# Kernel optimization log

Measured on AMD Instinct MI355X. Metric: run time of the kernel, lower is better.

## Reference

```python
import jax, jax.numpy as jnp
import numpy as np

N = 100000   # nodes
E = 1600000  # edges
D = 128      # in_dim
H = 128      # hidden_dim
C = 40       # num_classes
EPS = 1e-5   # LayerNorm eps (torch default)


def setup_inputs() -> dict:
    key = jax.random.key(0)
    ks = jax.random.split(key, 16)
    x = jax.random.normal(ks[0], (N, D), dtype=jnp.float32)
    edge_index = jax.random.randint(ks[1], (2, E), 0, N, dtype=jnp.int64)
    s = 1.0 / np.sqrt(D)
    inp = {"x": x, "edge_index": edge_index}
    # 3 GCN layers: weight [in, H], bias [H]; LayerNorm gamma/beta [H]
    for i in range(3):
        inp[f"W{i}"] = jax.random.normal(ks[2 + i], (D if i == 0 else H, H), dtype=jnp.float32) * s
        inp[f"b{i}"] = jnp.zeros((H,), jnp.float32)
        inp[f"g{i}"] = jnp.ones((H,), jnp.float32)
        inp[f"be{i}"] = jnp.zeros((H,), jnp.float32)
    inp["Wc"] = jax.random.normal(ks[10], (H, C), dtype=jnp.float32) * (1.0 / np.sqrt(H))
    inp["bc"] = jnp.zeros((C,), jnp.float32)
    return inp


def _layer_norm(h, g, b):
    mu = jnp.mean(h, axis=-1, keepdims=True)
    var = jnp.var(h, axis=-1, keepdims=True)  # biased, matches torch
    return (h - mu) * jax.lax.rsqrt(var + EPS) * g + b


def _gcn_conv(x, W, b, src, dst, enorm, dinv2):
    # GCNConv: D^{-1/2}(A+I)D^{-1/2} X W + b (self-loops handled analytically)
    h = x @ W                                   # [N, H]
    agg = jax.ops.segment_sum(h[src] * enorm[:, None], dst, num_segments=N)
    return agg + h * dinv2[:, None] + b


def reference(x, edge_index, W0, b0, g0, be0, W1, b1, g1, be1, W2, b2, g2, be2, Wc, bc):
    src, dst = edge_index[0], edge_index[1]
    # degree with self-loops (GCNConv adds self-loops by default)
    deg = jnp.zeros((N,), x.dtype).at[dst].add(1.0) + 1.0
    dinv = jax.lax.rsqrt(deg)
    enorm = dinv[src] * dinv[dst]               # per-edge normalization
    dinv2 = dinv * dinv                         # self-loop normalization

    Ws, bs, gs, bes = (W0, W1, W2), (b0, b1, b2), (g0, g1, g2), (be0, be1, be2)
    for i in range(3):
        x_in = x
        x = _gcn_conv(x, Ws[i], bs[i], src, dst, enorm, dinv2)
        x = _layer_norm(x, gs[i], bes[i])
        x = jax.nn.elu(x)
        if i > 0:
            x = x + x_in
        # dropout: eval mode / p=0 -> identity
    return x @ Wc + bc
```

## Files before the change

### kernel.cpp

```cpp
#include <hip/hip_runtime.h>
#include <math.h>

#define N_NODES 100000
#define N_EDGES 1600000
#define DIM     128
#define NCLS    40
#define NBUCK   196
#define P1_CH   4096
#define P1_GRID 391

typedef _Float16 f16x8 __attribute__((ext_vector_type(8)));
typedef _Float16 f16x2 __attribute__((ext_vector_type(2)));
typedef float    f32x4 __attribute__((ext_vector_type(4)));

__device__ inline unsigned short f16bits(float f) {
    union { _Float16 h; unsigned short u; } cv;
    cv.h = (_Float16)f;
    return cv.u;
}
__device__ inline f16x2 as_h2(unsigned u) {
    union { unsigned u; f16x2 h; } cv;
    cv.u = u;
    return cv.h;
}
__device__ inline unsigned as_u(f16x2 h) {
    union { f16x2 h; unsigned u; } cv;
    cv.h = h;
    return cv.u;
}
__device__ inline unsigned pack_h2(float lo, float hi) {
    f16x2 h;
    h.x = (_Float16)lo;
    h.y = (_Float16)hi;
    return as_u(h);
}

__global__ __launch_bounds__(256) void setup_misc(const float* __restrict__ W0,
                                                  const float* __restrict__ W1,
                                                  const float* __restrict__ W2,
                                                  const float* __restrict__ Wc,
                                                  unsigned short* __restrict__ Wsw0,
                                                  unsigned short* __restrict__ Wsw1,
                                                  unsigned short* __restrict__ Wsw2,
                                                  unsigned short* __restrict__ Wcsw,
                                                  int* __restrict__ bcnt) {
    int blk = blockIdx.x;
    if (blk < 192) {
        const float* W = (blk < 64) ? W0 : (blk < 128) ? W1 : W2;
        unsigned short* Wsw = (blk < 64) ? Wsw0 : (blk < 128) ? Wsw1 : Wsw2;
        int o = (blk & 63) * 256 + threadIdx.x;
        int f = o >> 9;
        int l = (o >> 3) & 63;
        int j = o & 7;
        int n = f >> 2;
        int s = f & 3;
        int k = s * 32 + (l >> 4) * 8 + j;
        int c = (l & 15) * 8 + n;
        Wsw[o] = f16bits(W[k * DIM + c]);
    } else if (blk < 216) {
        int o = (blk - 192) * 256 + threadIdx.x;
        int f = o >> 9;
        int l = (o >> 3) & 63;
        int j = o & 7;
        int n = f >> 2;
        int s = f & 3;
        int k = s * 32 + (l >> 4) * 8 + j;
        int c = (l & 15) * 3 + n;
        Wcsw[o] = (c < NCLS) ? f16bits(Wc[k * NCLS + c]) : (unsigned short)0;
    } else {
        bcnt[threadIdx.x] = 0;
    }
}

__global__ __launch_bounds__(256) void bhist(const int* __restrict__ ei,
                                             int* __restrict__ bcnt) {
    __shared__ int h[256];
    const int t  = threadIdx.x;
    const int e0 = blockIdx.x * P1_CH;
    const int cnt = min(P1_CH, N_EDGES - e0);
    h[t] = 0;
    __syncthreads();
    for (int i = t; i < cnt; i += 256)
        atomicAdd(&h[ei[N_EDGES + e0 + i] >> 9], 1);
    __syncthreads();
    if (h[t]) atomicAdd(&bcnt[t], h[t]);
}

__global__ __launch_bounds__(256) void bscan(const int* __restrict__ bcnt,
                                             int* __restrict__ bbase,
                                             int* __restrict__ bcur) {
    __shared__ int s[256];
    int t = threadIdx.x;
    s[t] = (t < NBUCK) ? bcnt[t] : 0;
    __syncthreads();
    for (int off = 1; off < 256; off <<= 1) {
        int x = (t >= off) ? s[t - off] : 0;
        __syncthreads();
        s[t] += x;
        __syncthreads();
    }
    int excl = (t == 0) ? 0 : s[t - 1];
    if (t < NBUCK) {
        bbase[t] = excl;
        bcur[t]  = excl;
    }
    if (t == 0) bbase[NBUCK] = N_EDGES;
}

__global__ __launch_bounds__(256) void bucket_p1(const int* __restrict__ ei,
                                                 int* __restrict__ bcur,
                                                 int2* __restrict__ tmp) {
    __shared__ int  hist[256];
    __shared__ int  lscan[256];
    __shared__ int  rank[256];
    __shared__ int  gbase[256];
    __shared__ int2 stage[P1_CH];
    const int t  = threadIdx.x;
    const int e0 = blockIdx.x * P1_CH;
    const int cnt = min(P1_CH, N_EDGES - e0);

    hist[t] = 0;
    __syncthreads();

    int2 ed[16];
#pragma unroll
    for (int i = 0; i < 16; ++i) {
        int idx = t + i * 256;
        if (idx < cnt) {
            int s = ei[e0 + idx];
            int d = ei[N_EDGES + e0 + idx];
            ed[i] = make_int2(s, d);
            atomicAdd(&hist[d >> 9], 1);
        }
    }
    __syncthreads();

    int hv = hist[t];
    lscan[t] = hv;
    __syncthreads();
    for (int off = 1; off < 256; off <<= 1) {
        int x = (t >= off) ? lscan[t - off] : 0;
        __syncthreads();
        lscan[t] += x;
        __syncthreads();
    }
    int excl = (t == 0) ? 0 : lscan[t - 1];
    __syncthreads();
    lscan[t] = excl;
    rank[t]  = excl;
    if (hv > 0) gbase[t] = atomicAdd(&bcur[t], hv);
    __syncthreads();

#pragma unroll
    for (int i = 0; i < 16; ++i) {
        int idx = t + i * 256;
        if (idx < cnt) {
            int b = ed[i].y >> 9;
            int p = atomicAdd(&rank[b], 1);
            stage[p] = ed[i];
        }
    }
    __syncthreads();

    for (int p = t; p < cnt; p += 256) {
        int2 v = stage[p];
        int b = v.y >> 9;
        tmp[gbase[b] + (p - lscan[b])] = v;
    }
}

__global__ __launch_bounds__(256) void bucket_p2a(const int2* __restrict__ tmp,
                                                  const int* __restrict__ bbase,
                                                  int* __restrict__ rowptr,
                                                  float* __restrict__ dinv) {
    __shared__ int cnt[512];
    __shared__ int pscan[256];
    const int t  = threadIdx.x;
    const int b  = blockIdx.x;
    const int d0 = b << 9;
    const int dend = min(d0 + 512, N_NODES);
    const int nn = dend - d0;

    cnt[t] = 0;
    cnt[t + 256] = 0;
    __syncthreads();

    const int beg = bbase[b];
    const int end = bbase[b + 1];
    for (int idx = beg + t; idx < end; idx += 256)
        atomicAdd(&cnt[tmp[idx].y - d0], 1);
    __syncthreads();

    int c0 = cnt[2 * t];
    int c1 = cnt[2 * t + 1];
    pscan[t] = c0 + c1;
    __syncthreads();
    for (int off = 1; off < 256; off <<= 1) {
        int x = (t >= off) ? pscan[t - off] : 0;
        __syncthreads();
        pscan[t] += x;
        __syncthreads();
    }
    int excl = (t == 0) ? 0 : pscan[t - 1];
    if (2 * t < nn) {
        rowptr[d0 + 2 * t] = beg + excl;
        dinv[d0 + 2 * t]   = rsqrtf((float)c0 + 1.0f);
    }
    if (2 * t + 1 < nn) {
        rowptr[d0 + 2 * t + 1] = beg + excl + c0;
        dinv[d0 + 2 * t + 1]   = rsqrtf((float)c1 + 1.0f);
    }
    if (b == NBUCK - 1 && t == 0) rowptr[N_NODES] = N_EDGES;
}

__global__ __launch_bounds__(256) void bucket_p2b(const int2* __restrict__ tmp,
                                                  const int* __restrict__ rowptr,
                                                  const float* __restrict__ dinv,
                                                  int2* __restrict__ rec) {
    __shared__ int cur[512];
    const int t  = threadIdx.x;
    const int b  = blockIdx.x;
    const int d0 = b << 9;
    const int dend = min(d0 + 512, N_NODES);
    const int nn = dend - d0;

    for (int i = t; i < nn; i += 256) cur[i] = rowptr[d0 + i];
    __syncthreads();

    const int beg = rowptr[d0];
    const int end = rowptr[dend];
    for (int idx = beg + t; idx < end; idx += 256) {
        int2 v = tmp[idx];
        int s = v.x, d = v.y;
        int pos = atomicAdd(&cur[d - d0], 1);
        unsigned short wb = f16bits(dinv[s] * dinv[d]);
        rec[pos] = make_int2(s << 8, (int)((unsigned)wb | ((unsigned)wb << 16)));
    }
}

__global__ __launch_bounds__(256, 2) void gemm_mfma_f(const float* __restrict__ X,
                                                      const unsigned short* __restrict__ Wsw,
                                                      unsigned short* __restrict__ H) {
    __shared__ unsigned short wlds[32 * 512];
    const int tid   = threadIdx.x;
    const int lane  = tid & 63;
    const int wave  = tid >> 6;
    const int row0w = blockIdx.x * 128 + wave * 32;
    const int m = lane & 15;
    const int q = lane >> 4;

    {
        const uint4* srcp = (const uint4*)Wsw;
        uint4*       dstp = (uint4*)wlds;
#pragma unroll
        for (int i = 0; i < 8; ++i) dstp[tid + i * 256] = srcp[tid + i * 256];
    }
    __syncthreads();

    f16x8 wf[32];
#pragma unroll
    for (int f = 0; f < 32; ++f)
        wf[f] = *(const f16x8*)(wlds + (f << 9) + lane * 8);

    f16x8 af[2][4];
#pragma unroll
    for (int ggr = 0; ggr < 2; ++ggr) {
        int r = row0w + ggr * 16 + m;
        if (r >= N_NODES) r = N_NODES - 1;
        const float* xp = X + (size_t)r * DIM + q * 8;
#pragma unroll
        for (int s = 0; s < 4; ++s) {
            float4 x0 = *(const float4*)(xp + s * 32);
            float4 x1 = *(const float4*)(xp + s * 32 + 4);
            f16x8 v;
            v[0] = (_Float16)x0.x; v[1] = (_Float16)x0.y;
            v[2] = (_Float16)x0.z; v[3] = (_Float16)x0.w;
            v[4] = (_Float16)x1.x; v[5] = (_Float16)x1.y;
            v[6] = (_Float16)x1.z; v[7] = (_Float16)x1.w;
            af[ggr][s] = v;
        }
    }

    f32x4 acc[2][8];
    f32x4 z = {0.f, 0.f, 0.f, 0.f};
#pragma unroll
    for (int ggr = 0; ggr < 2; ++ggr)
#pragma unroll
        for (int n = 0; n < 8; ++n) acc[ggr][n] = z;

#pragma unroll
    for (int s = 0; s < 4; ++s)
#pragma unroll
        for (int n = 0; n < 8; ++n) {
            acc[0][n] = __builtin_amdgcn_mfma_f32_16x16x32_f16(af[0][s], wf[n * 4 + s], acc[0][n], 0, 0, 0);
            acc[1][n] = __builtin_amdgcn_mfma_f32_16x16x32_f16(af[1][s], wf[n * 4 + s], acc[1][n], 0, 0, 0);
        }

#pragma unroll
    for (int ggr = 0; ggr < 2; ++ggr)
#pragma unroll
        for (int j = 0; j < 4; ++j) {
            int row = row0w + ggr * 16 + q * 4 + j;
            if (row < N_NODES) {
                uint4 o;
                o.x = pack_h2(acc[ggr][0][j], acc[ggr][1][j]);
                o.y = pack_h2(acc[ggr][2][j], acc[ggr][3][j]);
                o.z = pack_h2(acc[ggr][4][j], acc[ggr][5][j]);
                o.w = pack_h2(acc[ggr][6][j], acc[ggr][7][j]);
                *(uint4*)(H + (size_t)row * DIM + m * 8) = o;
            }
        }
}

__global__ __launch_bounds__(256, 2) void gemm_mfma_h(const unsigned short* __restrict__ Xh,
                                                      const unsigned short* __restrict__ Wsw,
                                                      unsigned short* __restrict__ H) {
    __shared__ unsigned short wlds[32 * 512];
    const int tid   = threadIdx.x;
    const int lane  = tid & 63;
    const int wave  = tid >> 6;
    const int row0w = blockIdx.x * 128 + wave * 32;
    const int m = lane & 15;
    const int q = lane >> 4;

    {
        const uint4* srcp = (const uint4*)Wsw;
        uint4*       dstp = (uint4*)wlds;
#pragma unroll
        for (int i = 0; i < 8; ++i) dstp[tid + i * 256] = srcp[tid + i * 256];
    }
    __syncthreads();

    f16x8 wf[32];
#pragma unroll
    for (int f = 0; f < 32; ++f)
        wf[f] = *(const f16x8*)(wlds + (f << 9) + lane * 8);

    f16x8 af[2][4];
#pragma unroll
    for (int ggr = 0; ggr < 2; ++ggr) {
        int r = row0w + ggr * 16 + m;
        if (r >= N_NODES) r = N_NODES - 1;
        const unsigned short* xp = Xh + (size_t)r * DIM + q * 8;
#pragma unroll
        for (int s = 0; s < 4; ++s) af[ggr][s] = *(const f16x8*)(xp + s * 32);
    }

    f32x4 acc[2][8];
    f32x4 z = {0.f, 0.f, 0.f, 0.f};
#pragma unroll
    for (int ggr = 0; ggr < 2; ++ggr)
#pragma unroll
        for (int n = 0; n < 8; ++n) acc[ggr][n] = z;

#pragma unroll
    for (int s = 0; s < 4; ++s)
#pragma unroll
        for (int n = 0; n < 8; ++n) {
            acc[0][n] = __builtin_amdgcn_mfma_f32_16x16x32_f16(af[0][s], wf[n * 4 + s], acc[0][n], 0, 0, 0);
            acc[1][n] = __builtin_amdgcn_mfma_f32_16x16x32_f16(af[1][s], wf[n * 4 + s], acc[1][n], 0, 0, 0);
        }

#pragma unroll
    for (int ggr = 0; ggr < 2; ++ggr)
#pragma unroll
        for (int j = 0; j < 4; ++j) {
            int row = row0w + ggr * 16 + q * 4 + j;
            if (row < N_NODES) {
                uint4 o;
                o.x = pack_h2(acc[ggr][0][j], acc[ggr][1][j]);
                o.y = pack_h2(acc[ggr][2][j], acc[ggr][3][j]);
                o.z = pack_h2(acc[ggr][4][j], acc[ggr][5][j]);
                o.w = pack_h2(acc[ggr][6][j], acc[ggr][7][j]);
                *(uint4*)(H + (size_t)row * DIM + m * 8) = o;
            }
        }
}

__global__ __launch_bounds__(256) void agg_ln(const unsigned short* __restrict__ Hh,
                                              const unsigned short* __restrict__ xin,
                                              const float* __restrict__ dinv,
                                              const float* __restrict__ bias,
                                              const float* __restrict__ g,
                                              const float* __restrict__ be,
                                              const int* __restrict__ rowptr,
                                              const int2* __restrict__ rec,
                                              unsigned short* __restrict__ outb) {
    int node = blockIdx.x * 4 + (threadIdx.x >> 6);
    int lane = threadIdx.x & 63;
    int sub  = lane & 15;
    int qtr  = lane >> 4;
    int beg = rowptr[node];
    int end = rowptr[node + 1];
    const char* Hb8 = (const char*)Hh;
    const unsigned laneoff = (unsigned)sub * 16;

    f16x2 acc[4];
    f16x2 hz = {(_Float16)0.f, (_Float16)0.f};
#pragma unroll
    for (int k = 0; k < 4; ++k) acc[k] = hz;

    for (int e0 = beg; e0 < end; e0 += 64) {
        int cnt = min(end - e0, 64);
        int2 rc = (lane < cnt) ? rec[e0 + lane] : make_int2(0, 0);
        int sv = rc.x;
        int wv = rc.y;
        int cntR = (cnt + 15) & ~15;
        for (int j = 0; j < cntR; j += 16) {
            int i0 = j + qtr, i1 = j + 4 + qtr, i2 = j + 8 + qtr, i3 = j + 12 + qtr;
            unsigned o0 = (unsigned)__shfl(sv, i0, 64) + laneoff;
            int      w0 = __shfl(wv, i0, 64);
            unsigned o1 = (unsigned)__shfl(sv, i1, 64) + laneoff;
            int      w1 = __shfl(wv, i1, 64);
            unsigned o2 = (unsigned)__shfl(sv, i2, 64) + laneoff;
            int      w2 = __shfl(wv, i2, 64);
            unsigned o3 = (unsigned)__shfl(sv, i3, 64) + laneoff;
            int      w3 = __shfl(wv, i3, 64);
            uint4 u0 = *(const uint4*)(Hb8 + o0);
            uint4 u1 = *(const uint4*)(Hb8 + o1);
            uint4 u2 = *(const uint4*)(Hb8 + o2);
            uint4 u3 = *(const uint4*)(Hb8 + o3);
            f16x2 hw0 = as_h2(w0), hw1 = as_h2(w1), hw2 = as_h2(w2), hw3 = as_h2(w3);
            acc[0] += as_h2(u0.x) * hw0;
            acc[1] += as_h2(u0.y) * hw0;
            acc[2] += as_h2(u0.z) * hw0;
            acc[3] += as_h2(u0.w) * hw0;
            acc[0] += as_h2(u1.x) * hw1;
            acc[1] += as_h2(u1.y) * hw1;
            acc[2] += as_h2(u1.z) * hw1;
            acc[3] += as_h2(u1.w) * hw1;
            acc[0] += as_h2(u2.x) * hw2;
            acc[1] += as_h2(u2.y) * hw2;
            acc[2] += as_h2(u2.z) * hw2;
            acc[3] += as_h2(u2.w) * hw2;
            acc[0] += as_h2(u3.x) * hw3;
            acc[1] += as_h2(u3.y) * hw3;
            acc[2] += as_h2(u3.z) * hw3;
            acc[3] += as_h2(u3.w) * hw3;
        }
    }

#pragma unroll
    for (int k = 0; k < 4; ++k) {
        acc[k] += as_h2(__shfl_xor(as_u(acc[k]), 16, 64));
        acc[k] += as_h2(__shfl_xor(as_u(acc[k]), 32, 64));
    }

    unsigned mu = as_u(acc[0]);
    mu = (qtr == 1) ? as_u(acc[1]) : mu;
    mu = (qtr == 2) ? as_u(acc[2]) : mu;
    mu = (qtr == 3) ? as_u(acc[3]) : mu;
    f16x2 mine = as_h2(mu);
    const int c0 = sub * 8 + qtr * 2;
    const unsigned nodeoff = ((unsigned)node << 8) + (unsigned)c0 * 2;

    float dv = dinv[node];
    float d2 = dv * dv;
    f16x2 hh = as_h2(*(const unsigned*)(Hb8 + nodeoff));
    float2 bb = *(const float2*)(bias + c0);
    float a0 = (float)mine.x + (float)hh.x * d2 + bb.x;
    float a1 = (float)mine.y + (float)hh.y * d2 + bb.y;

    float s1 = a0 + a1;
    float s2 = a0 * a0 + a1 * a1;
#pragma unroll
    for (int mk = 1; mk <= 32; mk <<= 1) {
        s1 += __shfl_xor(s1, mk, 64);
        s2 += __shfl_xor(s2, mk, 64);
    }
    float mean = s1 * (1.0f / 128.0f);
    float var  = s2 * (1.0f / 128.0f) - mean * mean;
    float rr   = rsqrtf(var + 1e-5f);
    float2 gg = *(const float2*)(g + c0);
    float2 ee = *(const float2*)(be + c0);
    float r0 = (a0 - mean) * rr * gg.x + ee.x;
    float r1 = (a1 - mean) * rr * gg.y + ee.y;
    r0 = r0 > 0.0f ? r0 : expm1f(r0);
    r1 = r1 > 0.0f ? r1 : expm1f(r1);
    if (xin) {
        f16x2 xi = as_h2(*(const unsigned*)((const char*)xin + nodeoff));
        r0 += (float)xi.x;
        r1 += (float)xi.y;
    }
    *(unsigned*)((char*)outb + nodeoff) = pack_h2(r0, r1);
}

__global__ __launch_bounds__(256) void classifier_mfma(const unsigned short* __restrict__ Xh,
                                                       const unsigned short* __restrict__ Wcsw,
                                                       const float* __restrict__ bc,
                                                       float* __restrict__ out) {
    __shared__ unsigned short wlds[12 * 512];
    const int tid   = threadIdx.x;
    const int lane  = tid & 63;
    const int wave  = tid >> 6;
    const int row0w = blockIdx.x * 128 + wave * 32;
    const int m = lane & 15;
    const int q = lane >> 4;

    {
        const uint4* srcp = (const uint4*)Wcsw;
        uint4*       dstp = (uint4*)wlds;
#pragma unroll
        for (int i = 0; i < 3; ++i) dstp[tid + i * 256] = srcp[tid + i * 256];
    }
    __syncthreads();

    f16x8 wf[12];
#pragma unroll
    for (int f = 0; f < 12; ++f)
        wf[f] = *(const f16x8*)(wlds + (f << 9) + lane * 8);

    f16x8 af[2][4];
#pragma unroll
    for (int ggr = 0; ggr < 2; ++ggr) {
        int r = row0w + ggr * 16 + m;
        if (r >= N_NODES) r = N_NODES - 1;
        const unsigned short* xp = Xh + (size_t)r * DIM + q * 8;
#pragma unroll
        for (int s = 0; s < 4; ++s) af[ggr][s] = *(const f16x8*)(xp + s * 32);
    }

    f32x4 acc[2][3];
    f32x4 z = {0.f, 0.f, 0.f, 0.f};
#pragma unroll
    for (int ggr = 0; ggr < 2; ++ggr)
#pragma unroll
        for (int n = 0; n < 3; ++n) acc[ggr][n] = z;

#pragma unroll
    for (int s = 0; s < 4; ++s)
#pragma unroll
        for (int n = 0; n < 3; ++n) {
            acc[0][n] = __builtin_amdgcn_mfma_f32_16x16x32_f16(af[0][s], wf[n * 4 + s], acc[0][n], 0, 0, 0);
            acc[1][n] = __builtin_amdgcn_mfma_f32_16x16x32_f16(af[1][s], wf[n * 4 + s], acc[1][n], 0, 0, 0);
        }

    float bcv[3];
#pragma unroll
    for (int n = 0; n < 3; ++n) {
        int c = 3 * m + n;
        bcv[n] = (c < NCLS) ? bc[c] : 0.f;
    }

#pragma unroll
    for (int ggr = 0; ggr < 2; ++ggr)
#pragma unroll
        for (int j = 0; j < 4; ++j) {
            int row = row0w + ggr * 16 + q * 4 + j;
            if (row < N_NODES) {
#pragma unroll
                for (int n = 0; n < 3; ++n) {
                    int c = 3 * m + n;
                    if (c < NCLS)
                        out[(size_t)row * NCLS + c] = acc[ggr][n][j] + bcv[n];
                }
            }
        }
}

extern "C" void kernel_launch(void* const* d_in, const int* in_sizes, int n_in,
                              void* d_out, int out_size, void* d_ws, size_t ws_size,
                              hipStream_t stream) {
    const float* x  = (const float*)d_in[0];
    const int*   ei = (const int*)d_in[1];
    const float* W[3]  = {(const float*)d_in[2], (const float*)d_in[6], (const float*)d_in[10]};
    const float* b[3]  = {(const float*)d_in[3], (const float*)d_in[7], (const float*)d_in[11]};
    const float* g[3]  = {(const float*)d_in[4], (const float*)d_in[8], (const float*)d_in[12]};
    const float* be[3] = {(const float*)d_in[5], (const float*)d_in[9], (const float*)d_in[13]};
    const float* Wc = (const float*)d_in[14];
    const float* bc = (const float*)d_in[15];
    float* out = (float*)d_out;

    char* ws = (char*)d_ws;
    const size_t NP = 400128;
    float* dinv   = (float*)(ws);
    int*   rowptr = (int*)  (ws + NP);
    int*   bcnt   = (int*)  (ws + 2 * NP);
    int*   bbase  = (int*)  (ws + 2 * NP + 1024);
    int*   bcur   = (int*)  (ws + 2 * NP + 2048);
    int2*  rec    = (int2*) (ws + 2 * NP + 4096);
    unsigned short* Hh = (unsigned short*)(ws + 2 * NP + 4096 + (size_t)N_EDGES * 8);
    unsigned short* Ah = Hh + (size_t)N_NODES * DIM;
    unsigned short* Ch = Ah + (size_t)N_NODES * DIM;
    unsigned short* Wsw0 = Ch + (size_t)N_NODES * DIM;
    unsigned short* Wsw1 = Wsw0 + DIM * DIM;
    unsigned short* Wsw2 = Wsw1 + DIM * DIM;
    unsigned short* Wcsw = Wsw2 + DIM * DIM;
    int2*  tmp    = (int2*)Ch;

    setup_misc<<<217, 256, 0, stream>>>(W[0], W[1], W[2], Wc, Wsw0, Wsw1, Wsw2, Wcsw, bcnt);

    bhist<<<P1_GRID, 256, 0, stream>>>(ei, bcnt);
    bscan<<<1, 256, 0, stream>>>(bcnt, bbase, bcur);
    bucket_p1<<<P1_GRID, 256, 0, stream>>>(ei, bcur, tmp);
    bucket_p2a<<<NBUCK, 256, 0, stream>>>(tmp, bbase, rowptr, dinv);
    bucket_p2b<<<NBUCK, 256, 0, stream>>>(tmp, rowptr, dinv, rec);

    const int gemm_grid = (N_NODES + 127) / 128;
    const int agg_grid  = N_NODES / 4;

    gemm_mfma_f<<<gemm_grid, 256, 0, stream>>>(x, Wsw0, Hh);
    agg_ln<<<agg_grid, 256, 0, stream>>>(Hh, nullptr, dinv, b[0], g[0], be[0], rowptr, rec, Ch);

    gemm_mfma_h<<<gemm_grid, 256, 0, stream>>>(Ch, Wsw1, Hh);
    agg_ln<<<agg_grid, 256, 0, stream>>>(Hh, Ch, dinv, b[1], g[1], be[1], rowptr, rec, Ah);

    gemm_mfma_h<<<gemm_grid, 256, 0, stream>>>(Ah, Wsw2, Hh);
    agg_ln<<<agg_grid, 256, 0, stream>>>(Hh, Ah, dinv, b[2], g[2], be[2], rowptr, rec, Ch);

    classifier_mfma<<<gemm_grid, 256, 0, stream>>>(Ch, Wcsw, bc, out);
}
```

Before: 425.5 us.

## Fold edge histogram into setup kernel and shrink GEMM tiles for occupancy

Merges the bucket histogram kernel into the weight-swizzle setup kernel, which saves one launch, and zeroes the counter with a memset instead. The GEMM kernels now process 16 rows per wave instead of 32 and read weight fragments from LDS inside the MFMA loop rather than holding all 32 in registers. This lowers register pressure so more waves can be resident, at the cost of more LDS reads and twice as many blocks each reloading the weights into LDS. The classifier grid is kept at its old size.

```diff
diff --git a/kernel.cpp b/kernel.cpp
--- a/kernel.cpp
+++ b/kernel.cpp
@@ -39,6 +39,7 @@
                                                   const float* __restrict__ W1,
                                                   const float* __restrict__ W2,
                                                   const float* __restrict__ Wc,
+                                                  const int* __restrict__ ei,
                                                   unsigned short* __restrict__ Wsw0,
                                                   unsigned short* __restrict__ Wsw1,
                                                   unsigned short* __restrict__ Wsw2,
@@ -68,22 +69,17 @@
         int c = (l & 15) * 3 + n;
         Wcsw[o] = (c < NCLS) ? f16bits(Wc[k * NCLS + c]) : (unsigned short)0;
     } else {
-        bcnt[threadIdx.x] = 0;
-    }
-}
-
-__global__ __launch_bounds__(256) void bhist(const int* __restrict__ ei,
-                                             int* __restrict__ bcnt) {
-    __shared__ int h[256];
-    const int t  = threadIdx.x;
-    const int e0 = blockIdx.x * P1_CH;
-    const int cnt = min(P1_CH, N_EDGES - e0);
-    h[t] = 0;
-    __syncthreads();
-    for (int i = t; i < cnt; i += 256)
-        atomicAdd(&h[ei[N_EDGES + e0 + i] >> 9], 1);
-    __syncthreads();
-    if (h[t]) atomicAdd(&bcnt[t], h[t]);
+        __shared__ int h[256];
+        const int t  = threadIdx.x;
+        const int e0 = (blk - 216) * P1_CH;
+        const int cnt = min(P1_CH, N_EDGES - e0);
+        h[t] = 0;
+        __syncthreads();
+        for (int i = t; i < cnt; i += 256)
+            atomicAdd(&h[ei[N_EDGES + e0 + i] >> 9], 1);
+        __syncthreads();
+        if (h[t]) atomicAdd(&bcnt[t], h[t]);
+    }
 }
 
 __global__ __launch_bounds__(256) void bscan(const int* __restrict__ bcnt,
@@ -238,14 +234,14 @@
     }
 }
 
-__global__ __launch_bounds__(256, 2) void gemm_mfma_f(const float* __restrict__ X,
-                                                      const unsigned short* __restrict__ Wsw,
-                                                      unsigned short* __restrict__ H) {
+__global__ __launch_bounds__(256) void gemm_mfma_f(const float* __restrict__ X,
+                                                   const unsigned short* __restrict__ Wsw,
+                                                   unsigned short* __restrict__ H) {
     __shared__ unsigned short wlds[32 * 512];
     const int tid   = threadIdx.x;
     const int lane  = tid & 63;
     const int wave  = tid >> 6;
-    const int row0w = blockIdx.x * 128 + wave * 32;
+    const int row0w = blockIdx.x * 64 + wave * 16;
     const int m = lane & 15;
     const int q = lane >> 4;
 
@@ -257,69 +253,58 @@
     }
     __syncthreads();
 
-    f16x8 wf[32];
-#pragma unroll
-    for (int f = 0; f < 32; ++f)
-        wf[f] = *(const f16x8*)(wlds + (f << 9) + lane * 8);
-
-    f16x8 af[2][4];
-#pragma unroll
-    for (int ggr = 0; ggr < 2; ++ggr) {
-        int r = row0w + ggr * 16 + m;
-        if (r >= N_NODES) r = N_NODES - 1;
-        const float* xp = X + (size_t)r * DIM + q * 8;
-#pragma unroll
-        for (int s = 0; s < 4; ++s) {
-            float4 x0 = *(const float4*)(xp + s * 32);
-            float4 x1 = *(const float4*)(xp + s * 32 + 4);
-            f16x8 v;
-            v[0] = (_Float16)x0.x; v[1] = (_Float16)x0.y;
-            v[2] = (_Float16)x0.z; v[3] = (_Float16)x0.w;
-            v[4] = (_Float16)x1.x; v[5] = (_Float16)x1.y;
-            v[6] = (_Float16)x1.z; v[7] = (_Float16)x1.w;
-            af[ggr][s] = v;
-        }
-    }
-
-    f32x4 acc[2][8];
+    int r = row0w + m;
+    if (r >= N_NODES) r = N_NODES - 1;
+    const float* xp = X + (size_t)r * DIM + q * 8;
+    f16x8 af[4];
+#pragma unroll
+    for (int s = 0; s < 4; ++s) {
+        float4 x0 = *(const float4*)(xp + s * 32);
+        float4 x1 = *(const float4*)(xp + s * 32 + 4);
+        f16x8 v;
+        v[0] = (_Float16)x0.x; v[1] = (_Float16)x0.y;
+        v[2] = (_Float16)x0.z; v[3] = (_Float16)x0.w;
+        v[4] = (_Float16)x1.x; v[5] = (_Float16)x1.y;
+        v[6] = (_Float16)x1.z; v[7] = (_Float16)x1.w;
+        af[s] = v;
+    }
+
+    f32x4 acc[8];
     f32x4 z = {0.f, 0.f, 0.f, 0.f};
 #pragma unroll
-    for (int ggr = 0; ggr < 2; ++ggr)
-#pragma unroll
-        for (int n = 0; n < 8; ++n) acc[ggr][n] = z;
-
+    for (int n = 0; n < 8; ++n) acc[n] = z;
+
+    const unsigned short* wl = wlds + lane * 8;
 #pragma unroll
     for (int s = 0; s < 4; ++s)
 #pragma unroll
         for (int n = 0; n < 8; ++n) {
-            acc[0][n] = __builtin_amdgcn_mfma_f32_16x16x32_f16(af[0][s], wf[n * 4 + s], acc[0][n], 0, 0, 0);
-            acc[1][n] = __builtin_amdgcn_mfma_f32_16x16x32_f16(af[1][s], wf[n * 4 + s], acc[1][n], 0, 0, 0);
-        }
-
-#pragma unroll
-    for (int ggr = 0; ggr < 2; ++ggr)
-#pragma unroll
-        for (int j = 0; j < 4; ++j) {
-            int row = row0w + ggr * 16 + q * 4 + j;
-            if (row < N_NODES) {
-                uint4 o;
-                o.x = pack_h2(acc[ggr][0][j], acc[ggr][1][j]);
-                o.y = pack_h2(acc[ggr][2][j], acc[ggr][3][j]);
-                o.z = pack_h2(acc[ggr][4][j], acc[ggr][5][j]);
-                o.w = pack_h2(acc[ggr][6][j], acc[ggr][7][j]);
-                *(uint4*)(H + (size_t)row * DIM + m * 8) = o;
-            }
-        }
-}
-
-__global__ __launch_bounds__(256, 2) void gemm_mfma_h(const unsigned short* __restrict__ Xh,
-                                                      const unsigned short* __restrict__ Wsw,
-                                                      unsigned short* __restrict__ H) {
+            f16x8 wf = *(const f16x8*)(wl + ((n * 4 + s) << 9));
+            acc[n] = __builtin_amdgcn_mfma_f32_16x16x32_f16(af[s], wf, acc[n], 0, 0, 0);
+        }
+
+#pragma unroll
+    for (int j = 0; j < 4; ++j) {
+        int row = row0w + q * 4 + j;
+        if (row < N_NODES) {
+            uint4 o;
+            o.x = pack_h2(acc[0][j], acc[1][j]);
+            o.y = pack_h2(acc[2][j], acc[3][j]);
+            o.z = pack_h2(acc[4][j], acc[5][j]);
+            o.w = pack_h2(acc[6][j], acc[7][j]);
+            *(uint4*)(H + (size_t)row * DIM + m * 8) = o;
+        }
+    }
+}
+
+__global__ __launch_bounds__(256) void gemm_mfma_h(const unsigned short* __restrict__ Xh,
+                                                   const unsigned short* __restrict__ Wsw,
+                                                   unsigned short* __restrict__ H) {
     __shared__ unsigned short wlds[32 * 512];
     const int tid   = threadIdx.x;
     const int lane  = tid & 63;
     const int wave  = tid >> 6;
-    const int row0w = blockIdx.x * 128 + wave * 32;
+    const int row0w = blockIdx.x * 64 + wave * 16;
     const int m = lane & 15;
     const int q = lane >> 4;
 
@@ -331,50 +316,39 @@
     }
     __syncthreads();
 
-    f16x8 wf[32];
-#pragma unroll
-    for (int f = 0; f < 32; ++f)
-        wf[f] = *(const f16x8*)(wlds + (f << 9) + lane * 8);
-
-    f16x8 af[2][4];
-#pragma unroll
-    for (int ggr = 0; ggr < 2; ++ggr) {
-        int r = row0w + ggr * 16 + m;
-        if (r >= N_NODES) r = N_NODES - 1;
-        const unsigned short* xp = Xh + (size_t)r * DIM + q * 8;
-#pragma unroll
-        for (int s = 0; s < 4; ++s) af[ggr][s] = *(const f16x8*)(xp + s * 32);
-    }
-
-    f32x4 acc[2][8];
+    int r = row0w + m;
+    if (r >= N_NODES) r = N_NODES - 1;
+    const unsigned short* xp = Xh + (size_t)r * DIM + q * 8;
+    f16x8 af[4];
+#pragma unroll
+    for (int s = 0; s < 4; ++s) af[s] = *(const f16x8*)(xp + s * 32);
+
+    f32x4 acc[8];
     f32x4 z = {0.f, 0.f, 0.f, 0.f};
 #pragma unroll
-    for (int ggr = 0; ggr < 2; ++ggr)
-#pragma unroll
-        for (int n = 0; n < 8; ++n) acc[ggr][n] = z;
-
+    for (int n = 0; n < 8; ++n) acc[n] = z;
+
+    const unsigned short* wl = wlds + lane * 8;
 #pragma unroll
     for (int s = 0; s < 4; ++s)
 #pragma unroll
         for (int n = 0; n < 8; ++n) {
-            acc[0][n] = __builtin_amdgcn_mfma_f32_16x16x32_f16(af[0][s], wf[n * 4 + s], acc[0][n], 0, 0, 0);
-            acc[1][n] = __builtin_amdgcn_mfma_f32_16x16x32_f16(af[1][s], wf[n * 4 + s], acc[1][n], 0, 0, 0);
-        }
-
-#pragma unroll
-    for (int ggr = 0; ggr < 2; ++ggr)
-#pragma unroll
-        for (int j = 0; j < 4; ++j) {
-            int row = row0w + ggr * 16 + q * 4 + j;
-            if (row < N_NODES) {
-                uint4 o;
-                o.x = pack_h2(acc[ggr][0][j], acc[ggr][1][j]);
-                o.y = pack_h2(acc[ggr][2][j], acc[ggr][3][j]);
-                o.z = pack_h2(acc[ggr][4][j], acc[ggr][5][j]);
-                o.w = pack_h2(acc[ggr][6][j], acc[ggr][7][j]);
-                *(uint4*)(H + (size_t)row * DIM + m * 8) = o;
-            }
-        }
+            f16x8 wf = *(const f16x8*)(wl + ((n * 4 + s) << 9));
+            acc[n] = __builtin_amdgcn_mfma_f32_16x16x32_f16(af[s], wf, acc[n], 0, 0, 0);
+        }
+
+#pragma unroll
+    for (int j = 0; j < 4; ++j) {
+        int row = row0w + q * 4 + j;
+        if (row < N_NODES) {
+            uint4 o;
+            o.x = pack_h2(acc[0][j], acc[1][j]);
+            o.y = pack_h2(acc[2][j], acc[3][j]);
+            o.z = pack_h2(acc[4][j], acc[5][j]);
+            o.w = pack_h2(acc[6][j], acc[7][j]);
+            *(uint4*)(H + (size_t)row * DIM + m * 8) = o;
+        }
+    }
 }
 
 __global__ __launch_bounds__(256) void agg_ln(const unsigned short* __restrict__ Hh,
@@ -588,15 +562,17 @@
     unsigned short* Wcsw = Wsw2 + DIM * DIM;
     int2*  tmp    = (int2*)Ch;
 
-    setup_misc<<<217, 256, 0, stream>>>(W[0], W[1], W[2], Wc, Wsw0, Wsw1, Wsw2, Wcsw, bcnt);
-
-    bhist<<<P1_GRID, 256, 0, stream>>>(ei, bcnt);
+    hipMemsetAsync(bcnt, 0, 1024, stream);
+    setup_misc<<<216 + P1_GRID, 256, 0, stream>>>(W[0], W[1], W[2], Wc, ei,
+                                                  Wsw0, Wsw1, Wsw2, Wcsw, bcnt);
+
     bscan<<<1, 256, 0, stream>>>(bcnt, bbase, bcur);
     bucket_p1<<<P1_GRID, 256, 0, stream>>>(ei, bcur, tmp);
     bucket_p2a<<<NBUCK, 256, 0, stream>>>(tmp, bbase, rowptr, dinv);
     bucket_p2b<<<NBUCK, 256, 0, stream>>>(tmp, rowptr, dinv, rec);
 
-    const int gemm_grid = (N_NODES + 127) / 128;
+    const int gemm_grid = (N_NODES + 63) / 64;
+    const int cls_grid  = (N_NODES + 127) / 128;
     const int agg_grid  = N_NODES / 4;
 
     gemm_mfma_f<<<gemm_grid, 256, 0, stream>>>(x, Wsw0, Hh);
@@ -608,5 +584,5 @@
     gemm_mfma_h<<<gemm_grid, 256, 0, stream>>>(Ah, Wsw2, Hh);
     agg_ln<<<agg_grid, 256, 0, stream>>>(Hh, Ah, dinv, b[2], g[2], be[2], rowptr, rec, Ch);
 
-    classifier_mfma<<<gemm_grid, 256, 0, stream>>>(Ch, Wcsw, bc, out);
-}
+    classifier_mfma<<<cls_grid, 256, 0, stream>>>(Ch, Wcsw, bc, out);
+}
```

Result: no change. 425.9 us (+0.1%).
